# Performance work log

Measured on AMD Instinct MI355X. Metric: run time of the kernel, lower is better.

The kernel has to match this reference:

```python
import jax, jax.numpy as jnp
import numpy as np

N_NODES = 100000
N_EDGES = 1600000
IN_DIM = 128
HID_DIM = 128


def gcn_conv(x, W, b, src, dst, n_nodes):
    # PyG GCNConv: linear (no bias) -> symmetric degree norm with self-loops -> scatter-add -> +bias
    h = x @ W  # [N, H]
    e = src.shape[0]
    deg = jax.ops.segment_sum(jnp.ones((e,), dtype=h.dtype), dst, num_segments=n_nodes) + 1.0  # +1 self-loop
    dinv = deg ** -0.5  # deg >= 1 always
    norm = dinv[src] * dinv[dst]  # [E]
    agg = jax.ops.segment_sum(h[src] * norm[:, None], dst, num_segments=n_nodes)
    agg = agg + h * (dinv * dinv)[:, None]  # self-loop contribution
    return agg + b


def setup_inputs() -> dict:
    key = jax.random.key(0)
    ks = jax.random.split(key, 8)
    x = jax.random.normal(ks[0], (N_NODES, IN_DIM), dtype=jnp.float32)
    edge_index = jax.random.randint(ks[1], (2, N_EDGES), 0, N_NODES, dtype=jnp.int32)
    def glorot(k, fan_in, fan_out):
        lim = np.sqrt(6.0 / (fan_in + fan_out)).astype(np.float32)
        return jax.random.uniform(k, (fan_in, fan_out), dtype=jnp.float32, minval=-lim, maxval=lim)
    W1 = glorot(ks[2], IN_DIM, HID_DIM)
    W2 = glorot(ks[3], HID_DIM, HID_DIM)
    W3 = glorot(ks[4], HID_DIM, HID_DIM)
    b1 = jnp.zeros((HID_DIM,), jnp.float32)
    b2 = jnp.zeros((HID_DIM,), jnp.float32)
    b3 = jnp.zeros((HID_DIM,), jnp.float32)
    return {"x": x, "W1": W1, "b1": b1, "W2": W2, "b2": b2, "W3": W3, "b3": b3,
            "edge_index": edge_index}


def reference(x, W1, b1, W2, b2, W3, b3, edge_index):
    src, dst = edge_index[0], edge_index[1]
    n = x.shape[0]
    z = jax.nn.relu(gcn_conv(x, W1, b1, src, dst, n))
    z = jax.nn.relu(gcn_conv(z, W2, b2, src, dst, n))
    z = gcn_conv(z, W3, b3, src, dst, n)
    # edge dot-product decode on the same edge set
    logits = jnp.sum(z[src] * z[dst], axis=1)  # [E]
    return jax.nn.sigmoid(logits)
```

## Files before the change

### kernel.cpp

```cpp
#include <hip/hip_runtime.h>
#include <math.h>

#define NN 100000
#define NE 1600000
#define DIM 128
#define SCHUNK 1024

typedef unsigned short u16;
typedef unsigned int u32;
typedef __attribute__((ext_vector_type(8))) short bf16x8;
typedef __attribute__((ext_vector_type(4))) float f32x4;

__device__ inline u16 f2bf(float f) {
  union { float f; u32 u; } v; v.f = f;
  u32 r = v.u + 0x7FFF + ((v.u >> 16) & 1);
  return (u16)(r >> 16);
}
__device__ inline float bflo(u32 u) { union { u32 u; float f; } v; v.u = u << 16; return v.f; }
__device__ inline float bfhi(u32 u) { union { u32 u; float f; } v; v.u = u & 0xFFFF0000u; return v.f; }

__global__ void k_deg(const int* __restrict__ dst, int* __restrict__ deg) {
  int i = blockIdx.x * blockDim.x + threadIdx.x;
  if (i < NE) atomicAdd(&deg[dst[i]], 1);
}

__global__ void k_dinv(const int* __restrict__ deg, float* __restrict__ dinv) {
  int i = blockIdx.x * blockDim.x + threadIdx.x;
  if (i < NN) dinv[i] = rsqrtf((float)deg[i] + 1.0f);
}

__global__ void k_scan1(const int* __restrict__ deg, int* __restrict__ bsum) {
  __shared__ int sd[256];
  int t = threadIdx.x;
  int base = blockIdx.x * SCHUNK + t * 4;
  int s = 0;
#pragma unroll
  for (int j = 0; j < 4; ++j) { int idx = base + j; if (idx < NN) s += deg[idx]; }
  sd[t] = s; __syncthreads();
  for (int off = 128; off > 0; off >>= 1) {
    if (t < off) sd[t] += sd[t + off];
    __syncthreads();
  }
  if (t == 0) bsum[blockIdx.x] = sd[0];
}

__global__ void k_scan2(int* __restrict__ bsum, int nb) {
  if (threadIdx.x == 0 && blockIdx.x == 0) {
    int run = 0;
    for (int b = 0; b < nb; ++b) { int v = bsum[b]; bsum[b] = run; run += v; }
  }
}

__global__ void k_scan3(const int* __restrict__ deg, const int* __restrict__ bsum,
                        int* __restrict__ offs) {
  __shared__ int ts[256];
  int t = threadIdx.x;
  int base = blockIdx.x * SCHUNK + t * 4;
  int v[4]; int loc = 0;
#pragma unroll
  for (int j = 0; j < 4; ++j) { int idx = base + j; v[j] = (idx < NN) ? deg[idx] : 0; loc += v[j]; }
  ts[t] = loc; __syncthreads();
  for (int off = 1; off < 256; off <<= 1) {
    int x = (t >= off) ? ts[t - off] : 0;
    __syncthreads();
    ts[t] += x;
    __syncthreads();
  }
  int run = bsum[blockIdx.x] + ts[t] - loc;
#pragma unroll
  for (int j = 0; j < 4; ++j) { int idx = base + j; if (idx < NN) offs[idx] = run; run += v[j]; }
}

__global__ void k_fill(const int* __restrict__ src, const int* __restrict__ dst,
                       const int* __restrict__ offs, int* __restrict__ cur,
                       uint2* __restrict__ csr_se) {
  int i = blockIdx.x * blockDim.x + threadIdx.x;
  if (i < NE) {
    int d = dst[i];
    int pos = offs[d] + atomicAdd(&cur[d], 1);
    csr_se[pos] = make_uint2((u32)src[i], (u32)i);
  }
}

__global__ void k_tobf(const float* __restrict__ in, u16* __restrict__ out, int n4) {
  int i = blockIdx.x * blockDim.x + threadIdx.x;
  if (i < n4) {
    float4 v = ((const float4*)in)[i];
    ushort4 o;
    o.x = f2bf(v.x); o.y = f2bf(v.y); o.z = f2bf(v.z); o.w = f2bf(v.w);
    ((ushort4*)out)[i] = o;
  }
}

__global__ void k_pack(const float* __restrict__ W, u16* __restrict__ Wp) {
  int tid = blockIdx.x * blockDim.x + threadIdx.x;
  int b = tid & 7, j = (tid >> 3) & 15, kb = (tid >> 7) & 3, ks = (tid >> 9) & 3, ct = tid >> 11;
  int k = ks * 32 + kb * 8 + b, col = ct * 16 + j;
  Wp[tid] = f2bf(W[k * 128 + col]);
}

__launch_bounds__(256)
__global__ void k_gemm(const u16* __restrict__ Xb, const u16* __restrict__ Wp,
                       const float* __restrict__ dinv, u16* __restrict__ hp) {
  __shared__ u16 wl[16384];
  __shared__ u16 ctile[4][2048];
  int t = threadIdx.x;
  int w = t >> 6, l = t & 63;
  int row0 = blockIdx.x * 64;
  int rbase = row0 + w * 16;

#pragma unroll
  for (int i = 0; i < 8; ++i) {
    int off = (i * 256 + t) * 8;
    *(uint4*)&wl[off] = *(const uint4*)&Wp[off];
  }
  __syncthreads();

  int arow = rbase + (l & 15);
  arow = arow < NN ? arow : NN - 1;
  const u16* abase = Xb + (size_t)arow * DIM + (l >> 4) * 8;
  bf16x8 a[4];
#pragma unroll
  for (int ks = 0; ks < 4; ++ks) a[ks] = *(const bf16x8*)(abase + ks * 32);

  f32x4 acc[8];
#pragma unroll
  for (int ct = 0; ct < 8; ++ct) {
    acc[ct] = (f32x4){0.f, 0.f, 0.f, 0.f};
#pragma unroll
    for (int ks = 0; ks < 4; ++ks) {
      bf16x8 bfr = *(const bf16x8*)&wl[ct * 2048 + ks * 512 + (l >> 4) * 128 + (l & 15) * 8];
      acc[ct] = __builtin_amdgcn_mfma_f32_16x16x32_bf16(a[ks], bfr, acc[ct], 0, 0, 0);
    }
  }

  float dv[4];
#pragma unroll
  for (int v = 0; v < 4; ++v) {
    int rr = rbase + (l >> 4) * 4 + v;
    dv[v] = dinv[rr < NN ? rr : NN - 1];
  }
  u16* ct_lds = ctile[w];
#pragma unroll
  for (int ct = 0; ct < 8; ++ct) {
#pragma unroll
    for (int v = 0; v < 4; ++v) {
      int row = (l >> 4) * 4 + v;
      ct_lds[row * DIM + ct * 16 + (l & 15)] = f2bf(dv[v] * acc[ct][v]);
    }
  }
  __syncthreads();
#pragma unroll
  for (int rr = 0; rr < 4; ++rr) {
    int row = rr * 4 + (l >> 4);
    int grow = rbase + row;
    if (grow < NN)
      *(uint4*)&hp[(size_t)grow * DIM + (l & 15) * 8] =
          *(const uint4*)&ct_lds[row * DIM + (l & 15) * 8];
  }
}

__launch_bounds__(256)
__global__ void k_agg(const u16* __restrict__ hp, const uint2* __restrict__ csr_se,
                      const int* __restrict__ offs, const int* __restrict__ deg,
                      const float* __restrict__ dinv, const float* __restrict__ bias,
                      u16* __restrict__ outb, int relu) {
  int t = threadIdx.x;
  int g = t >> 5, l = t & 31;
  int n = blockIdx.x * 8 + g;
  float dn = dinv[n];
  int s = offs[n], cnt = deg[n];
  const uint2* hp2 = (const uint2*)hp;
  float a0 = 0.f, a1 = 0.f, a2 = 0.f, a3 = 0.f;
  int i = 0;
  for (; i + 4 <= cnt; i += 4) {
    int u0 = csr_se[s + i].x;
    int u1 = csr_se[s + i + 1].x;
    int u2 = csr_se[s + i + 2].x;
    int u3 = csr_se[s + i + 3].x;
    uint2 v0 = hp2[(size_t)u0 * 32 + l];
    uint2 v1 = hp2[(size_t)u1 * 32 + l];
    uint2 v2 = hp2[(size_t)u2 * 32 + l];
    uint2 v3 = hp2[(size_t)u3 * 32 + l];
    a0 += (bflo(v0.x) + bflo(v1.x)) + (bflo(v2.x) + bflo(v3.x));
    a1 += (bfhi(v0.x) + bfhi(v1.x)) + (bfhi(v2.x) + bfhi(v3.x));
    a2 += (bflo(v0.y) + bflo(v1.y)) + (bflo(v2.y) + bflo(v3.y));
    a3 += (bfhi(v0.y) + bfhi(v1.y)) + (bfhi(v2.y) + bfhi(v3.y));
  }
  for (; i < cnt; ++i) {
    int u = csr_se[s + i].x;
    uint2 v = hp2[(size_t)u * 32 + l];
    a0 += bflo(v.x); a1 += bfhi(v.x); a2 += bflo(v.y); a3 += bfhi(v.y);
  }
  uint2 sv = hp2[(size_t)n * 32 + l];
  float4 bb = ((const float4*)bias)[l];
  float r0 = dn * (a0 + bflo(sv.x)) + bb.x;
  float r1 = dn * (a1 + bfhi(sv.x)) + bb.y;
  float r2 = dn * (a2 + bflo(sv.y)) + bb.z;
  float r3 = dn * (a3 + bfhi(sv.y)) + bb.w;
  if (relu) {
    r0 = fmaxf(r0, 0.f); r1 = fmaxf(r1, 0.f);
    r2 = fmaxf(r2, 0.f); r3 = fmaxf(r3, 0.f);
  }
  ushort4 o; o.x = f2bf(r0); o.y = f2bf(r1); o.z = f2bf(r2); o.w = f2bf(r3);
  *(ushort4*)&outb[(size_t)n * DIM + l * 4] = o;
}

__device__ inline float sigm(float x) { return 1.0f / (1.0f + expf(-x)); }

__launch_bounds__(256)
__global__ void k_decode_node(const u16* __restrict__ z, const uint2* __restrict__ csr_se,
                              const int* __restrict__ offs, const int* __restrict__ deg,
                              float* __restrict__ out) {
  int t = threadIdx.x;
  int g = t >> 5, l = t & 31;
  int n = blockIdx.x * 8 + g;
  const uint2* z2 = (const uint2*)z;
  uint2 zn = z2[(size_t)n * 32 + l];
  float n0 = bflo(zn.x), n1 = bfhi(zn.x), n2 = bflo(zn.y), n3 = bfhi(zn.y);
  int s = offs[n], cnt = deg[n];
  int i = 0;
  for (; i + 4 <= cnt; i += 4) {
    uint2 e0 = csr_se[s + i];
    uint2 e1 = csr_se[s + i + 1];
    uint2 e2 = csr_se[s + i + 2];
    uint2 e3 = csr_se[s + i + 3];
    uint2 v0 = z2[(size_t)e0.x * 32 + l];
    uint2 v1 = z2[(size_t)e1.x * 32 + l];
    uint2 v2 = z2[(size_t)e2.x * 32 + l];
    uint2 v3 = z2[(size_t)e3.x * 32 + l];
    float p0 = bflo(v0.x) * n0 + bfhi(v0.x) * n1 + bflo(v0.y) * n2 + bfhi(v0.y) * n3;
    float p1 = bflo(v1.x) * n0 + bfhi(v1.x) * n1 + bflo(v1.y) * n2 + bfhi(v1.y) * n3;
    float p2 = bflo(v2.x) * n0 + bfhi(v2.x) * n1 + bflo(v2.y) * n2 + bfhi(v2.y) * n3;
    float p3 = bflo(v3.x) * n0 + bfhi(v3.x) * n1 + bflo(v3.y) * n2 + bfhi(v3.y) * n3;
#pragma unroll
    for (int off = 16; off >= 1; off >>= 1) {
      p0 += __shfl_xor(p0, off);
      p1 += __shfl_xor(p1, off);
      p2 += __shfl_xor(p2, off);
      p3 += __shfl_xor(p3, off);
    }
    if (l == 0) {
      out[e0.y] = sigm(p0);
      out[e1.y] = sigm(p1);
      out[e2.y] = sigm(p2);
      out[e3.y] = sigm(p3);
    }
  }
  for (; i < cnt; ++i) {
    uint2 e = csr_se[s + i];
    uint2 v = z2[(size_t)e.x * 32 + l];
    float p = bflo(v.x) * n0 + bfhi(v.x) * n1 + bflo(v.y) * n2 + bfhi(v.y) * n3;
#pragma unroll
    for (int off = 16; off >= 1; off >>= 1) p += __shfl_xor(p, off);
    if (l == 0) out[e.y] = sigm(p);
  }
}

extern "C" void kernel_launch(void* const* d_in, const int* in_sizes, int n_in,
                              void* d_out, int out_size, void* d_ws, size_t ws_size,
                              hipStream_t stream) {
  const float* x  = (const float*)d_in[0];
  const float* W1 = (const float*)d_in[1];
  const float* b1 = (const float*)d_in[2];
  const float* W2 = (const float*)d_in[3];
  const float* b2 = (const float*)d_in[4];
  const float* W3 = (const float*)d_in[5];
  const float* b3 = (const float*)d_in[6];
  const int*   ei = (const int*)d_in[7];
  const int* src = ei;
  const int* dst = ei + NE;
  float* out = (float*)d_out;

  char* w = (char*)d_ws;
  size_t p = 0;
  auto alloc = [&](size_t bytes) -> void* {
    void* r = w + p;
    p += (bytes + 255) & ~(size_t)255;
    return r;
  };
  int*   deg     = (int*)alloc((size_t)NN * 4);
  int*   cur     = (int*)alloc((size_t)NN * 4);
  int*   offs    = (int*)alloc((size_t)NN * 4);
  float* dinv    = (float*)alloc((size_t)NN * 4);
  int*   bsum    = (int*)alloc(1024);
  uint2* csr_se  = (uint2*)alloc((size_t)NE * 8);
  u16*   Xb      = (u16*)alloc((size_t)NN * DIM * 2);
  u16*   hp      = (u16*)alloc((size_t)NN * DIM * 2);
  u16*   hb      = (u16*)alloc((size_t)NN * DIM * 2);
  u16*   Wp1     = (u16*)alloc(16384 * 2);
  u16*   Wp2     = (u16*)alloc(16384 * 2);
  u16*   Wp3     = (u16*)alloc(16384 * 2);
  (void)in_sizes; (void)n_in; (void)out_size; (void)ws_size;

  hipMemsetAsync(deg, 0, (size_t)NN * 4, stream);
  hipMemsetAsync(cur, 0, (size_t)NN * 4, stream);

  k_deg<<<(NE + 255) / 256, 256, 0, stream>>>(dst, deg);
  k_dinv<<<(NN + 255) / 256, 256, 0, stream>>>(deg, dinv);
  int nb = (NN + SCHUNK - 1) / SCHUNK;
  k_scan1<<<nb, 256, 0, stream>>>(deg, bsum);
  k_scan2<<<1, 64, 0, stream>>>(bsum, nb);
  k_scan3<<<nb, 256, 0, stream>>>(deg, bsum, offs);
  k_fill<<<(NE + 255) / 256, 256, 0, stream>>>(src, dst, offs, cur, csr_se);

  k_tobf<<<(NN * DIM / 4 + 255) / 256, 256, 0, stream>>>(x, Xb, NN * DIM / 4);
  k_pack<<<64, 256, 0, stream>>>(W1, Wp1);
  k_pack<<<64, 256, 0, stream>>>(W2, Wp2);
  k_pack<<<64, 256, 0, stream>>>(W3, Wp3);

  int gb = (NN + 63) / 64;
  k_gemm<<<gb, 256, 0, stream>>>(Xb, Wp1, dinv, hp);
  k_agg <<<NN / 8, 256, 0, stream>>>(hp, csr_se, offs, deg, dinv, b1, hb, 1);
  k_gemm<<<gb, 256, 0, stream>>>(hb, Wp2, dinv, hp);
  k_agg <<<NN / 8, 256, 0, stream>>>(hp, csr_se, offs, deg, dinv, b2, hb, 1);
  k_gemm<<<gb, 256, 0, stream>>>(hb, Wp3, dinv, hp);
  k_agg <<<NN / 8, 256, 0, stream>>>(hp, csr_se, offs, deg, dinv, b3, hb, 0);

  k_decode_node<<<NN / 8, 256, 0, stream>>>(hb, csr_se, offs, deg, out);
}
```

Before: 527.5 us.

## Build CSR via two-pass bucketed sort and split src/edge-id arrays

Replaces the single-pass atomic scatter CSR fill with a two-stage bucket sort. The first pass groups edges into 256-node buckets using shared-memory counting and staging before doing chunked global writes. The second pass places each edge within its bucket using shared-memory atomics. The packed (src, eid) array is also split into separate arrays, so the three aggregation passes read only 4-byte source indices; the cost is an extra kernel, a staging buffer, and per-bucket copies done by a single thread each.

```diff
diff --git a/kernel.cpp b/kernel.cpp
--- a/kernel.cpp
+++ b/kernel.cpp
@@ -5,6 +5,8 @@
 #define NE 1600000
 #define DIM 128
 #define SCHUNK 1024
+#define NBK 391
+#define ECH 4096
 
 typedef unsigned short u16;
 typedef unsigned int u32;
@@ -71,14 +73,82 @@
   for (int j = 0; j < 4; ++j) { int idx = base + j; if (idx < NN) offs[idx] = run; run += v[j]; }
 }
 
-__global__ void k_fill(const int* __restrict__ src, const int* __restrict__ dst,
-                       const int* __restrict__ offs, int* __restrict__ cur,
-                       uint2* __restrict__ csr_se) {
-  int i = blockIdx.x * blockDim.x + threadIdx.x;
-  if (i < NE) {
-    int d = dst[i];
-    int pos = offs[d] + atomicAdd(&cur[d], 1);
-    csr_se[pos] = make_uint2((u32)src[i], (u32)i);
+__launch_bounds__(256)
+__global__ void k_bucket(const int* __restrict__ src, const int* __restrict__ dst,
+                         const int* __restrict__ offs, int* __restrict__ bcur,
+                         uint2* __restrict__ bstage) {
+  __shared__ int cnt[512];
+  __shared__ int bl[512];
+  __shared__ int gb[512];
+  __shared__ int tmp[256];
+  __shared__ uint2 st[ECH];
+  int t = threadIdx.x;
+  int e0 = blockIdx.x * ECH;
+  cnt[t] = 0; cnt[t + 256] = 0;
+  __syncthreads();
+  int b_[16], r_[16]; u32 s_[16], y_[16];
+#pragma unroll
+  for (int k = 0; k < 16; ++k) {
+    int i = e0 + k * 256 + t;
+    b_[k] = -1;
+    if (i < NE) {
+      int d = dst[i];
+      int bb = d >> 8;
+      b_[k] = bb;
+      s_[k] = (u32)src[i];
+      y_[k] = ((u32)(d & 255) << 21) | (u32)i;
+      r_[k] = atomicAdd(&cnt[bb], 1);
+    }
+  }
+  __syncthreads();
+  int c0 = cnt[2 * t], c1 = cnt[2 * t + 1];
+  tmp[t] = c0 + c1;
+  __syncthreads();
+  for (int off = 1; off < 256; off <<= 1) {
+    int v = (t >= off) ? tmp[t - off] : 0;
+    __syncthreads();
+    tmp[t] += v;
+    __syncthreads();
+  }
+  int excl = tmp[t] - (c0 + c1);
+  bl[2 * t] = excl; bl[2 * t + 1] = excl + c0;
+  __syncthreads();
+#pragma unroll
+  for (int k = 0; k < 16; ++k)
+    if (b_[k] >= 0) st[bl[b_[k]] + r_[k]] = make_uint2(s_[k], y_[k]);
+  for (int b = t; b < 512; b += 256) {
+    int n = cnt[b];
+    gb[b] = (n > 0) ? atomicAdd(&bcur[b], n) : 0;
+  }
+  __syncthreads();
+  for (int b = t; b < 512; b += 256) {
+    int n = cnt[b];
+    if (n > 0) {
+      uint2* dp = bstage + offs[b << 8] + gb[b];
+      const uint2* sp = st + bl[b];
+      for (int j = 0; j < n; ++j) dp[j] = sp[j];
+    }
+  }
+}
+
+__launch_bounds__(256)
+__global__ void k_fillb(const uint2* __restrict__ bstage, const int* __restrict__ offs,
+                        int* __restrict__ csr_src, int* __restrict__ csr_eid) {
+  __shared__ int curl[256];
+  int t = threadIdx.x;
+  int b = blockIdx.x;
+  int nb0 = b << 8;
+  curl[t] = 0;
+  __syncthreads();
+  int sbase = offs[nb0];
+  int send = (b == NBK - 1) ? NE : offs[nb0 + 256];
+  for (int j = sbase + t; j < send; j += 256) {
+    uint2 e = bstage[j];
+    int dl = e.y >> 21;
+    int eid = e.y & 0x1FFFFF;
+    int pos = offs[nb0 + dl] + atomicAdd(&curl[dl], 1);
+    csr_src[pos] = (int)e.x;
+    csr_eid[pos] = eid;
   }
 }
 
@@ -161,7 +231,7 @@
 }
 
 __launch_bounds__(256)
-__global__ void k_agg(const u16* __restrict__ hp, const uint2* __restrict__ csr_se,
+__global__ void k_agg(const u16* __restrict__ hp, const int* __restrict__ csr_src,
                       const int* __restrict__ offs, const int* __restrict__ deg,
                       const float* __restrict__ dinv, const float* __restrict__ bias,
                       u16* __restrict__ outb, int relu) {
@@ -174,10 +244,10 @@
   float a0 = 0.f, a1 = 0.f, a2 = 0.f, a3 = 0.f;
   int i = 0;
   for (; i + 4 <= cnt; i += 4) {
-    int u0 = csr_se[s + i].x;
-    int u1 = csr_se[s + i + 1].x;
-    int u2 = csr_se[s + i + 2].x;
-    int u3 = csr_se[s + i + 3].x;
+    int u0 = csr_src[s + i];
+    int u1 = csr_src[s + i + 1];
+    int u2 = csr_src[s + i + 2];
+    int u3 = csr_src[s + i + 3];
     uint2 v0 = hp2[(size_t)u0 * 32 + l];
     uint2 v1 = hp2[(size_t)u1 * 32 + l];
     uint2 v2 = hp2[(size_t)u2 * 32 + l];
@@ -188,7 +258,7 @@
     a3 += (bfhi(v0.y) + bfhi(v1.y)) + (bfhi(v2.y) + bfhi(v3.y));
   }
   for (; i < cnt; ++i) {
-    int u = csr_se[s + i].x;
+    int u = csr_src[s + i];
     uint2 v = hp2[(size_t)u * 32 + l];
     a0 += bflo(v.x); a1 += bfhi(v.x); a2 += bflo(v.y); a3 += bfhi(v.y);
   }
@@ -209,9 +279,9 @@
 __device__ inline float sigm(float x) { return 1.0f / (1.0f + expf(-x)); }
 
 __launch_bounds__(256)
-__global__ void k_decode_node(const u16* __restrict__ z, const uint2* __restrict__ csr_se,
-                              const int* __restrict__ offs, const int* __restrict__ deg,
-                              float* __restrict__ out) {
+__global__ void k_decode_node(const u16* __restrict__ z, const int* __restrict__ csr_src,
+                              const int* __restrict__ csr_eid, const int* __restrict__ offs,
+                              const int* __restrict__ deg, float* __restrict__ out) {
   int t = threadIdx.x;
   int g = t >> 5, l = t & 31;
   int n = blockIdx.x * 8 + g;
@@ -221,14 +291,14 @@
   int s = offs[n], cnt = deg[n];
   int i = 0;
   for (; i + 4 <= cnt; i += 4) {
-    uint2 e0 = csr_se[s + i];
-    uint2 e1 = csr_se[s + i + 1];
-    uint2 e2 = csr_se[s + i + 2];
-    uint2 e3 = csr_se[s + i + 3];
-    uint2 v0 = z2[(size_t)e0.x * 32 + l];
-    uint2 v1 = z2[(size_t)e1.x * 32 + l];
-    uint2 v2 = z2[(size_t)e2.x * 32 + l];
-    uint2 v3 = z2[(size_t)e3.x * 32 + l];
+    int u0 = csr_src[s + i];
+    int u1 = csr_src[s + i + 1];
+    int u2 = csr_src[s + i + 2];
+    int u3 = csr_src[s + i + 3];
+    uint2 v0 = z2[(size_t)u0 * 32 + l];
+    uint2 v1 = z2[(size_t)u1 * 32 + l];
+    uint2 v2 = z2[(size_t)u2 * 32 + l];
+    uint2 v3 = z2[(size_t)u3 * 32 + l];
     float p0 = bflo(v0.x) * n0 + bfhi(v0.x) * n1 + bflo(v0.y) * n2 + bfhi(v0.y) * n3;
     float p1 = bflo(v1.x) * n0 + bfhi(v1.x) * n1 + bflo(v1.y) * n2 + bfhi(v1.y) * n3;
     float p2 = bflo(v2.x) * n0 + bfhi(v2.x) * n1 + bflo(v2.y) * n2 + bfhi(v2.y) * n3;
@@ -241,19 +311,19 @@
       p3 += __shfl_xor(p3, off);
     }
     if (l == 0) {
-      out[e0.y] = sigm(p0);
-      out[e1.y] = sigm(p1);
-      out[e2.y] = sigm(p2);
-      out[e3.y] = sigm(p3);
+      out[csr_eid[s + i]]     = sigm(p0);
+      out[csr_eid[s + i + 1]] = sigm(p1);
+      out[csr_eid[s + i + 2]] = sigm(p2);
+      out[csr_eid[s + i + 3]] = sigm(p3);
     }
   }
   for (; i < cnt; ++i) {
-    uint2 e = csr_se[s + i];
-    uint2 v = z2[(size_t)e.x * 32 + l];
+    int u = csr_src[s + i];
+    uint2 v = z2[(size_t)u * 32 + l];
     float p = bflo(v.x) * n0 + bfhi(v.x) * n1 + bflo(v.y) * n2 + bfhi(v.y) * n3;
 #pragma unroll
     for (int off = 16; off >= 1; off >>= 1) p += __shfl_xor(p, off);
-    if (l == 0) out[e.y] = sigm(p);
+    if (l == 0) out[csr_eid[s + i]] = sigm(p);
   }
 }
 
@@ -280,11 +350,13 @@
     return r;
   };
   int*   deg     = (int*)alloc((size_t)NN * 4);
-  int*   cur     = (int*)alloc((size_t)NN * 4);
   int*   offs    = (int*)alloc((size_t)NN * 4);
   float* dinv    = (float*)alloc((size_t)NN * 4);
   int*   bsum    = (int*)alloc(1024);
-  uint2* csr_se  = (uint2*)alloc((size_t)NE * 8);
+  int*   bcur    = (int*)alloc(512 * 4);
+  uint2* bstage  = (uint2*)alloc((size_t)NE * 8);
+  int*   csr_src = (int*)alloc((size_t)NE * 4);
+  int*   csr_eid = (int*)alloc((size_t)NE * 4);
   u16*   Xb      = (u16*)alloc((size_t)NN * DIM * 2);
   u16*   hp      = (u16*)alloc((size_t)NN * DIM * 2);
   u16*   hb      = (u16*)alloc((size_t)NN * DIM * 2);
@@ -294,7 +366,7 @@
   (void)in_sizes; (void)n_in; (void)out_size; (void)ws_size;
 
   hipMemsetAsync(deg, 0, (size_t)NN * 4, stream);
-  hipMemsetAsync(cur, 0, (size_t)NN * 4, stream);
+  hipMemsetAsync(bcur, 0, 512 * 4, stream);
 
   k_deg<<<(NE + 255) / 256, 256, 0, stream>>>(dst, deg);
   k_dinv<<<(NN + 255) / 256, 256, 0, stream>>>(deg, dinv);
@@ -302,7 +374,10 @@
   k_scan1<<<nb, 256, 0, stream>>>(deg, bsum);
   k_scan2<<<1, 64, 0, stream>>>(bsum, nb);
   k_scan3<<<nb, 256, 0, stream>>>(deg, bsum, offs);
-  k_fill<<<(NE + 255) / 256, 256, 0, stream>>>(src, dst, offs, cur, csr_se);
+
+  int cb = (NE + ECH - 1) / ECH;
+  k_bucket<<<cb, 256, 0, stream>>>(src, dst, offs, bcur, bstage);
+  k_fillb<<<NBK, 256, 0, stream>>>(bstage, offs, csr_src, csr_eid);
 
   k_tobf<<<(NN * DIM / 4 + 255) / 256, 256, 0, stream>>>(x, Xb, NN * DIM / 4);
   k_pack<<<64, 256, 0, stream>>>(W1, Wp1);
@@ -311,11 +386,11 @@
 
   int gb = (NN + 63) / 64;
   k_gemm<<<gb, 256, 0, stream>>>(Xb, Wp1, dinv, hp);
-  k_agg <<<NN / 8, 256, 0, stream>>>(hp, csr_se, offs, deg, dinv, b1, hb, 1);
+  k_agg <<<NN / 8, 256, 0, stream>>>(hp, csr_src, offs, deg, dinv, b1, hb, 1);
   k_gemm<<<gb, 256, 0, stream>>>(hb, Wp2, dinv, hp);
-  k_agg <<<NN / 8, 256, 0, stream>>>(hp, csr_se, offs, deg, dinv, b2, hb, 1);
+  k_agg <<<NN / 8, 256, 0, stream>>>(hp, csr_src, offs, deg, dinv, b2, hb, 1);
   k_gemm<<<gb, 256, 0, stream>>>(hb, Wp3, dinv, hp);
-  k_agg <<<NN / 8, 256, 0, stream>>>(hp, csr_se, offs, deg, dinv, b3, hb, 0);
-
-  k_decode_node<<<NN / 8, 256, 0, stream>>>(hb, csr_se, offs, deg, out);
-}
+  k_agg <<<NN / 8, 256, 0, stream>>>(hp, csr_src, offs, deg, dinv, b3, hb, 0);
+
+  k_decode_node<<<NN / 8, 256, 0, stream>>>(hb, csr_src, csr_eid, offs, deg, out);
+}
```

After: 475.3 us. -9.9%, faster.
